# Optimization experiments

Hardware: AMD Instinct MI355X
Metric: run time of the kernel (lower is better)

The kernel has to match this reference:

```python
import jax, jax.numpy as jnp
import numpy as np

INPUT_SIZE = 128
HID = 64
B, T = 256, 1024

def setup_inputs() -> dict:
    key = jax.random.key(0)
    ks = jax.random.split(key, 12)
    s1 = 1.0 / np.sqrt(HID)
    def u(k, shape):
        return jax.random.uniform(k, shape, jnp.float32, -s1, s1)
    return {
        "x": jax.random.normal(ks[0], (B, T, INPUT_SIZE), jnp.float32),
        "w_ih0": u(ks[1], (4 * HID, INPUT_SIZE)),
        "w_hh0": u(ks[2], (4 * HID, HID)),
        "b_ih0": u(ks[3], (4 * HID,)),
        "b_hh0": u(ks[4], (4 * HID,)),
        "w_ih1": u(ks[5], (4 * HID, HID)),
        "w_hh1": u(ks[6], (4 * HID, HID)),
        "b_ih1": u(ks[7], (4 * HID,)),
        "b_hh1": u(ks[8], (4 * HID,)),
        "w_out": u(ks[9], (1, HID)),
        "b_out": u(ks[10], (1,)),
    }

def _lstm(x, w_ih, w_hh, b_ih, b_hh):
    # x: [B, T, I] -> h sequence [B, T, H]; PyTorch gate order i, f, g, o
    Bb = x.shape[0]
    H = w_hh.shape[1]
    # precompute input contribution for all timesteps (one big GEMM)
    xg = jnp.einsum('bti,gi->btg', x, w_ih) + b_ih + b_hh  # [B, T, 4H]
    def step(carry, g_t):
        h, c = carry
        g = g_t + h @ w_hh.T  # [B, 4H]
        i, f, gg, o = jnp.split(g, 4, axis=-1)
        i = jax.nn.sigmoid(i)
        f = jax.nn.sigmoid(f)
        gg = jnp.tanh(gg)
        o = jax.nn.sigmoid(o)
        c = f * c + i * gg
        h = o * jnp.tanh(c)
        return (h, c), h
    init = (jnp.zeros((Bb, H), x.dtype), jnp.zeros((Bb, H), x.dtype))
    _, hs = jax.lax.scan(step, init, jnp.swapaxes(xg, 0, 1))  # [T, B, H]
    return jnp.swapaxes(hs, 0, 1)

def reference(x, w_ih0, w_hh0, b_ih0, b_hh0, w_ih1, w_hh1, b_ih1, b_hh1, w_out, b_out):
    h1 = _lstm(x, w_ih0, w_hh0, b_ih0, b_hh0)   # [B, T, H]
    h2 = _lstm(h1, w_ih1, w_hh1, b_ih1, b_hh1)  # [B, T, H]
    logits = jnp.einsum('bth,oh->bto', h2, w_out) + b_out  # [B, T, 1]
    return jax.nn.sigmoid(logits)
```

## Files before the change

kernel.cpp:

```cpp
#include <hip/hip_runtime.h>

#define BB 256
#define TT 1024
#define II 128
#define HH 64
#define BT (BB * TT)

typedef _Float16 h2 __attribute__((ext_vector_type(2)));
typedef _Float16 half8 __attribute__((ext_vector_type(8)));
typedef float f32x4 __attribute__((ext_vector_type(4)));
typedef unsigned int uint;
typedef unsigned short ushort;

#define DOT2(a, b, c) __builtin_amdgcn_fdot2((a), (b), (c), false)
#define BC(u) __builtin_bit_cast(h2, (uint)(u))
#define MFMA16(a, b, c) __builtin_amdgcn_mfma_f32_16x16x32_f16((a), (b), (c), 0, 0, 0)
#define SIG(v) __builtin_amdgcn_rcpf(1.0f + __expf(-(v)))
#define TNH(v) (1.0f - 2.0f * __builtin_amdgcn_rcpf(1.0f + __expf(2.0f * (v))))

#define BAR() asm volatile("s_waitcnt lgkmcnt(0)\n\ts_barrier" ::: "memory")

#define LDPK(P, ptr) uint P; { float2 _f = *(const float2*)(ptr); \
    h2 _h; _h[0] = (_Float16)_f.x; _h[1] = (_Float16)_f.y; \
    P = __builtin_bit_cast(uint, _h); }
#define PIN8(a,b,c,d,e,f,g,h_) asm volatile("" : "+v"(a),"+v"(b),"+v"(c),"+v"(d),"+v"(e),"+v"(f),"+v"(g),"+v"(h_));
#define LD8(P, base, o) \
    LDPK(P##0,(base)+(o)+ 0) LDPK(P##1,(base)+(o)+ 2) LDPK(P##2,(base)+(o)+ 4) LDPK(P##3,(base)+(o)+ 6) \
    LDPK(P##4,(base)+(o)+ 8) LDPK(P##5,(base)+(o)+10) LDPK(P##6,(base)+(o)+12) LDPK(P##7,(base)+(o)+14) \
    PIN8(P##0,P##1,P##2,P##3,P##4,P##5,P##6,P##7)

#define D8A(P, va, vb, c0, c1, c2, c3) \
    c0 = DOT2(BC(P##0), BC((va).x), c0); c1 = DOT2(BC(P##1), BC((va).y), c1); \
    c2 = DOT2(BC(P##2), BC((va).z), c2); c3 = DOT2(BC(P##3), BC((va).w), c3); \
    c0 = DOT2(BC(P##4), BC((vb).x), c0); c1 = DOT2(BC(P##5), BC((vb).y), c1); \
    c2 = DOT2(BC(P##6), BC((vb).z), c2); c3 = DOT2(BC(P##7), BC((vb).w), c3);

#define GDOT(G, s) { float a0=0.f,a1=0.f,a2=0.f,a3=0.f; \
    D8A(G##A, hv0, hv1, a0,a1,a2,a3) D8A(G##B, hv2, hv3, a0,a1,a2,a3) \
    D8A(G##C, hv4, hv5, a0,a1,a2,a3) D8A(G##D, hv6, hv7, a0,a1,a2,a3) \
    s = (a0 + a1) + (a2 + a3); }

__global__ __launch_bounds__(256)
void xg_mfma(const float* __restrict__ x, const float* __restrict__ w_ih0,
             ushort* __restrict__ xg)
{
    __shared__ __align__(16) _Float16 xt[64][136];
    __shared__ __align__(16) _Float16 wt[128][136];
    const int tid = threadIdx.x, lane = tid & 63, wv = tid >> 6;
    const int bt0 = blockIdx.x * 64;
    {
        const int row = tid >> 2, q = (tid & 3) * 32;
        const float4* src = (const float4*)(x + (size_t)(bt0 + row) * II + q);
        _Float16* dst = &xt[row][q];
        #pragma unroll
        for (int i = 0; i < 8; ++i) {
            float4 v = src[i];
            dst[4*i+0]=(_Float16)v.x; dst[4*i+1]=(_Float16)v.y;
            dst[4*i+2]=(_Float16)v.z; dst[4*i+3]=(_Float16)v.w;
        }
    }
    for (int nh = 0; nh < 2; ++nh) {
        __syncthreads();
        {
            const int n = tid >> 1, kh = (tid & 1) * 64;
            const float4* src = (const float4*)(w_ih0 + (size_t)(nh * 128 + n) * II + kh);
            _Float16* dst = &wt[n][kh];
            #pragma unroll
            for (int i = 0; i < 16; ++i) {
                float4 v = src[i];
                dst[4*i+0]=(_Float16)v.x; dst[4*i+1]=(_Float16)v.y;
                dst[4*i+2]=(_Float16)v.z; dst[4*i+3]=(_Float16)v.w;
            }
        }
        __syncthreads();
        const int m = wv * 16 + (lane & 15);
        const int kf = (lane >> 4) * 8;
        half8 a0 = *(const half8*)&xt[m][ 0 + kf];
        half8 a1 = *(const half8*)&xt[m][32 + kf];
        half8 a2 = *(const half8*)&xt[m][64 + kf];
        half8 a3 = *(const half8*)&xt[m][96 + kf];
        #pragma unroll
        for (int nt = 0; nt < 8; ++nt) {
            const int nloc = nt * 16 + (lane & 15);
            half8 b0 = *(const half8*)&wt[nloc][ 0 + kf];
            half8 b1 = *(const half8*)&wt[nloc][32 + kf];
            half8 b2 = *(const half8*)&wt[nloc][64 + kf];
            half8 b3 = *(const half8*)&wt[nloc][96 + kf];
            f32x4 acc = {0.f, 0.f, 0.f, 0.f};
            acc = MFMA16(a0, b0, acc); acc = MFMA16(a1, b1, acc);
            acc = MFMA16(a2, b2, acc); acc = MFMA16(a3, b3, acc);
            const int col = nh * 128 + nt * 16 + (lane & 15);
            const int idx = (col & 63) * 4 + (col >> 6);
            const int r0  = wv * 16 + (lane >> 4) * 4;
            #pragma unroll
            for (int r = 0; r < 4; ++r) {
                _Float16 hv = (_Float16)acc[r];
                xg[(size_t)(bt0 + r0 + r) * 256 + idx] = __builtin_bit_cast(ushort, hv);
            }
        }
    }
}

__global__ __launch_bounds__(192) __attribute__((amdgpu_waves_per_eu(1, 1)))
void lstm2_core(const float* __restrict__ w_hh0,
                const float* __restrict__ b_ih0, const float* __restrict__ b_hh0,
                const float* __restrict__ w_ih1, const float* __restrict__ w_hh1,
                const float* __restrict__ b_ih1, const float* __restrict__ b_hh1,
                const ushort* __restrict__ xg, ushort* __restrict__ h1g)
{
    const int bb = blockIdx.x;
    const int w  = threadIdx.x >> 6;
    const int j  = threadIdx.x & 63;

    __shared__ __align__(16) uint  h0buf[2][32];
    __shared__ __align__(16) uint  h1buf[2][32];
    __shared__ float zbuf[2][4][68];

    const float* Wsel = (w == 0) ? w_hh0 : (w == 1) ? w_ih1 : w_hh1;
    const float* r0p = Wsel + (size_t)(  0 + j) * 64;
    const float* r1p = Wsel + (size_t)( 64 + j) * 64;
    const float* r2p = Wsel + (size_t)(128 + j) * 64;
    const float* r3p = Wsel + (size_t)(192 + j) * 64;
    LD8(G0A, r0p,  0) LD8(G0B, r0p, 16) LD8(G0C, r0p, 32) LD8(G0D, r0p, 48)
    LD8(G1A, r1p,  0) LD8(G1B, r1p, 16) LD8(G1C, r1p, 32) LD8(G1D, r1p, 48)
    LD8(G2A, r2p,  0) LD8(G2B, r2p, 16) LD8(G2C, r2p, 32) LD8(G2D, r2p, 48)
    LD8(G3A, r3p,  0) LD8(G3B, r3p, 16) LD8(G3C, r3p, 32) LD8(G3D, r3p, 48)

    float bI = 0.f, bF = 0.f, bG = 0.f, bO = 0.f;
    if (w == 0) {
        bI = b_ih0[j]       + b_hh0[j];
        bF = b_ih0[64 + j]  + b_hh0[64 + j];
        bG = b_ih0[128 + j] + b_hh0[128 + j];
        bO = b_ih0[192 + j] + b_hh0[192 + j];
    } else if (w == 2) {
        bI = b_ih1[j]       + b_hh1[j];
        bF = b_ih1[64 + j]  + b_hh1[64 + j];
        bG = b_ih1[128 + j] + b_hh1[128 + j];
        bO = b_ih1[192 + j] + b_hh1[192 + j];
    }

    float cst = 0.0f;
    const ushort* xbase = xg + (size_t)bb * TT * 256 + j * 4;
    ushort* h1b = h1g + (size_t)bb * TT * 64 + j;

    if (threadIdx.x < 32)       h0buf[1][threadIdx.x] = 0u;
    else if (threadIdx.x < 64)  h1buf[1][threadIdx.x - 32] = 0u;
    __syncthreads();

    uint2 xc = {0,0}, xn1 = {0,0}, xn2 = {0,0};
    if (w == 0) {
        xc  = *(const uint2*)(xbase);
        xn1 = *(const uint2*)(xbase + 256);
    }

    for (int k = 0; k < TT + 2; ++k) {
        if (w == 0) {
            if (k + 2 < TT) xn2 = *(const uint2*)(xbase + (size_t)(k + 2) * 256);
            if (k < TT) {
                const uint4* hq = (const uint4*)&h0buf[(k + 1) & 1][0];
                uint4 hv0=hq[0], hv1=hq[1], hv2=hq[2], hv3=hq[3];
                uint4 hv4=hq[4], hv5=hq[5], hv6=hq[6], hv7=hq[7];
                float si, sf, sg, so;
                GDOT(G0, si) GDOT(G1, sf) GDOT(G2, sg) GDOT(G3, so)
                h2 xlo = BC(xc.x), xhi = BC(xc.y);
                si += bI + (float)xlo[0]; sf += bF + (float)xlo[1];
                sg += bG + (float)xhi[0]; so += bO + (float)xhi[1];
                float ii = SIG(si), ff = SIG(sf), gg = TNH(sg), oo = SIG(so);
                cst = fmaf(ff, cst, ii * gg);
                float hval = oo * TNH(cst);
                ((_Float16*)&h0buf[k & 1][0])[j] = (_Float16)hval;
            }
            xc = xn1; xn1 = xn2;
        } else if (w == 1) {
            if (k >= 1 && k <= TT) {
                const int m = k - 1;
                const uint4* hq = (const uint4*)&h0buf[m & 1][0];
                uint4 hv0=hq[0], hv1=hq[1], hv2=hq[2], hv3=hq[3];
                uint4 hv4=hq[4], hv5=hq[5], hv6=hq[6], hv7=hq[7];
                float si, sf, sg, so;
                GDOT(G0, si) GDOT(G1, sf) GDOT(G2, sg) GDOT(G3, so)
                const int s = m & 1;
                zbuf[s][0][j] = si; zbuf[s][1][j] = sf;
                zbuf[s][2][j] = sg; zbuf[s][3][j] = so;
            }
        } else {
            if (k >= 2) {
                const int m = k - 2;
                const int s = m & 1;
                const uint4* hq = (const uint4*)&h1buf[(m + 1) & 1][0];
                uint4 hv0=hq[0], hv1=hq[1], hv2=hq[2], hv3=hq[3];
                uint4 hv4=hq[4], hv5=hq[5], hv6=hq[6], hv7=hq[7];
                float si, sf, sg, so;
                GDOT(G0, si) GDOT(G1, sf) GDOT(G2, sg) GDOT(G3, so)
                si += bI + zbuf[s][0][j]; sf += bF + zbuf[s][1][j];
                sg += bG + zbuf[s][2][j]; so += bO + zbuf[s][3][j];
                float ii = SIG(si), ff = SIG(sf), gg = TNH(sg), oo = SIG(so);
                cst = fmaf(ff, cst, ii * gg);
                float hval = oo * TNH(cst);
                _Float16 hf = (_Float16)hval;
                ((_Float16*)&h1buf[m & 1][0])[j] = hf;
                h1b[(size_t)m * 64] = __builtin_bit_cast(ushort, hf);
            }
        }
        BAR();
    }
}

__global__ __launch_bounds__(256)
void head_gemv(const ushort* __restrict__ h1g, const float* __restrict__ w_out,
               const float* __restrict__ b_out, float* __restrict__ outp)
{
    __shared__ float wsh[64];
    const int tid = threadIdx.x;
    if (tid < 64) wsh[tid] = w_out[tid];
    __syncthreads();
    const int bt = blockIdx.x * 256 + tid;
    const uint4* hp = (const uint4*)(h1g + (size_t)bt * 64);
    float s = 0.0f;
    #pragma unroll
    for (int i = 0; i < 8; ++i) {
        uint4 v = hp[i];
        const float* wp = &wsh[8 * i];
        h2 p;
        p = BC(v.x); s = fmaf((float)p[0], wp[0], s); s = fmaf((float)p[1], wp[1], s);
        p = BC(v.y); s = fmaf((float)p[0], wp[2], s); s = fmaf((float)p[1], wp[3], s);
        p = BC(v.z); s = fmaf((float)p[0], wp[4], s); s = fmaf((float)p[1], wp[5], s);
        p = BC(v.w); s = fmaf((float)p[0], wp[6], s); s = fmaf((float)p[1], wp[7], s);
    }
    outp[bt] = __builtin_amdgcn_rcpf(1.0f + __expf(-(s + b_out[0])));
}

extern "C" void kernel_launch(void* const* d_in, const int* in_sizes, int n_in,
                              void* d_out, int out_size, void* d_ws, size_t ws_size,
                              hipStream_t stream) {
    const float* x     = (const float*)d_in[0];
    const float* w_ih0 = (const float*)d_in[1];
    const float* w_hh0 = (const float*)d_in[2];
    const float* b_ih0 = (const float*)d_in[3];
    const float* b_hh0 = (const float*)d_in[4];
    const float* w_ih1 = (const float*)d_in[5];
    const float* w_hh1 = (const float*)d_in[6];
    const float* b_ih1 = (const float*)d_in[7];
    const float* b_hh1 = (const float*)d_in[8];
    const float* w_out = (const float*)d_in[9];
    const float* b_out = (const float*)d_in[10];
    float* out = (float*)d_out;

    ushort* xg  = (ushort*)d_ws;
    ushort* h1g = (ushort*)((char*)d_ws + (size_t)BT * 256 * 2);

    hipLaunchKernelGGL(xg_mfma, dim3(BT / 64), dim3(256), 0, stream, x, w_ih0, xg);
    hipLaunchKernelGGL(lstm2_core, dim3(BB), dim3(192), 0, stream,
                       w_hh0, b_ih0, b_hh0, w_ih1, w_hh1, b_ih1, b_hh1, xg, h1g);
    hipLaunchKernelGGL(head_gemv, dim3(BT / 256), dim3(256), 0, stream,
                       h1g, w_out, b_out, out);
}
```

Baseline: 822.4 us.

## Prefetch hidden-state and gate vectors into registers across barriers in LSTM core

Restructures the three-wave LSTM pipeline so each wave issues its LDS loads of the next step's hidden vector (and the layer-1 input gates) right after writing, before the barrier. The loads complete under the barrier rather than after it, shortening the per-step critical path. It deepens the ring buffers to four slots, adds pipeline stages, uses partial lgkmcnt waits and barriers without waits per wave, and packs zbuf as float4 per unit. It also changes the xg layout by permuting w_ih0 rows so stores are contiguous. The relaxed waits risk LDS races if the counts or buffer slots are wrong.

```diff
diff --git a/kernel.cpp b/kernel.cpp
--- a/kernel.cpp
+++ b/kernel.cpp
@@ -18,7 +18,9 @@
 #define SIG(v) __builtin_amdgcn_rcpf(1.0f + __expf(-(v)))
 #define TNH(v) (1.0f - 2.0f * __builtin_amdgcn_rcpf(1.0f + __expf(2.0f * (v))))
 
-#define BAR() asm volatile("s_waitcnt lgkmcnt(0)\n\ts_barrier" ::: "memory")
+#define BAR_W8() asm volatile("s_waitcnt lgkmcnt(8)\n\ts_barrier" ::: "memory")
+#define BAR_W0() asm volatile("s_waitcnt lgkmcnt(0)\n\ts_barrier" ::: "memory")
+#define BAR_NP() asm volatile("s_barrier" ::: "memory")
 
 #define LDPK(P, ptr) uint P; { float2 _f = *(const float2*)(ptr); \
     h2 _h; _h[0] = (_Float16)_f.x; _h[1] = (_Float16)_f.y; \
@@ -39,6 +41,10 @@
     D8A(G##A, hv0, hv1, a0,a1,a2,a3) D8A(G##B, hv2, hv3, a0,a1,a2,a3) \
     D8A(G##C, hv4, hv5, a0,a1,a2,a3) D8A(G##D, hv6, hv7, a0,a1,a2,a3) \
     s = (a0 + a1) + (a2 + a3); }
+
+#define LDHV(src) { const uint4* hq_ = (const uint4*)(src); \
+    hv0=hq_[0]; hv1=hq_[1]; hv2=hq_[2]; hv3=hq_[3]; \
+    hv4=hq_[4]; hv5=hq_[5]; hv6=hq_[6]; hv7=hq_[7]; }
 
 __global__ __launch_bounds__(256)
 void xg_mfma(const float* __restrict__ x, const float* __restrict__ w_ih0,
@@ -63,7 +69,9 @@
         __syncthreads();
         {
             const int n = tid >> 1, kh = (tid & 1) * 64;
-            const float4* src = (const float4*)(w_ih0 + (size_t)(nh * 128 + n) * II + kh);
+            const int flatn = nh * 128 + n;
+            const int srcrow = (flatn & 3) * 64 + (flatn >> 2);
+            const float4* src = (const float4*)(w_ih0 + (size_t)srcrow * II + kh);
             _Float16* dst = &wt[n][kh];
             #pragma unroll
             for (int i = 0; i < 16; ++i) {
@@ -89,13 +97,12 @@
             f32x4 acc = {0.f, 0.f, 0.f, 0.f};
             acc = MFMA16(a0, b0, acc); acc = MFMA16(a1, b1, acc);
             acc = MFMA16(a2, b2, acc); acc = MFMA16(a3, b3, acc);
-            const int col = nh * 128 + nt * 16 + (lane & 15);
-            const int idx = (col & 63) * 4 + (col >> 6);
-            const int r0  = wv * 16 + (lane >> 4) * 4;
+            const int colg = nh * 128 + nt * 16 + (lane & 15);
+            const int r0   = wv * 16 + (lane >> 4) * 4;
             #pragma unroll
             for (int r = 0; r < 4; ++r) {
                 _Float16 hv = (_Float16)acc[r];
-                xg[(size_t)(bt0 + r0 + r) * 256 + idx] = __builtin_bit_cast(ushort, hv);
+                xg[(size_t)(bt0 + r0 + r) * 256 + colg] = __builtin_bit_cast(ushort, hv);
             }
         }
     }
@@ -112,9 +119,9 @@
     const int w  = threadIdx.x >> 6;
     const int j  = threadIdx.x & 63;
 
-    __shared__ __align__(16) uint  h0buf[2][32];
-    __shared__ __align__(16) uint  h1buf[2][32];
-    __shared__ float zbuf[2][4][68];
+    __shared__ __align__(16) uint  h0buf[4][32];
+    __shared__ __align__(16) uint  h1buf[32];
+    __shared__ __align__(16) float zbuf[4][64][4];
 
     const float* Wsel = (w == 0) ? w_hh0 : (w == 1) ? w_ih1 : w_hh1;
     const float* r0p = Wsel + (size_t)(  0 + j) * 64;
@@ -143,23 +150,19 @@
     const ushort* xbase = xg + (size_t)bb * TT * 256 + j * 4;
     ushort* h1b = h1g + (size_t)bb * TT * 64 + j;
 
-    if (threadIdx.x < 32)       h0buf[1][threadIdx.x] = 0u;
-    else if (threadIdx.x < 64)  h1buf[1][threadIdx.x - 32] = 0u;
-    __syncthreads();
-
+    uint4 hv0={0,0,0,0}, hv1={0,0,0,0}, hv2={0,0,0,0}, hv3={0,0,0,0};
+    uint4 hv4={0,0,0,0}, hv5={0,0,0,0}, hv6={0,0,0,0}, hv7={0,0,0,0};
+    f32x4 zr = {0.f, 0.f, 0.f, 0.f};
     uint2 xc = {0,0}, xn1 = {0,0}, xn2 = {0,0};
     if (w == 0) {
         xc  = *(const uint2*)(xbase);
         xn1 = *(const uint2*)(xbase + 256);
     }
 
-    for (int k = 0; k < TT + 2; ++k) {
+    for (int k = 0; k < TT + 4; ++k) {
         if (w == 0) {
             if (k + 2 < TT) xn2 = *(const uint2*)(xbase + (size_t)(k + 2) * 256);
             if (k < TT) {
-                const uint4* hq = (const uint4*)&h0buf[(k + 1) & 1][0];
-                uint4 hv0=hq[0], hv1=hq[1], hv2=hq[2], hv3=hq[3];
-                uint4 hv4=hq[4], hv5=hq[5], hv6=hq[6], hv7=hq[7];
                 float si, sf, sg, so;
                 GDOT(G0, si) GDOT(G1, sf) GDOT(G2, sg) GDOT(G3, so)
                 h2 xlo = BC(xc.x), xhi = BC(xc.y);
@@ -168,41 +171,41 @@
                 float ii = SIG(si), ff = SIG(sf), gg = TNH(sg), oo = SIG(so);
                 cst = fmaf(ff, cst, ii * gg);
                 float hval = oo * TNH(cst);
-                ((_Float16*)&h0buf[k & 1][0])[j] = (_Float16)hval;
+                ((_Float16*)&h0buf[k & 3][0])[j] = (_Float16)hval;
+                LDHV(&h0buf[k & 3][0]);
             }
             xc = xn1; xn1 = xn2;
+            BAR_W8();
         } else if (w == 1) {
-            if (k >= 1 && k <= TT) {
-                const int m = k - 1;
-                const uint4* hq = (const uint4*)&h0buf[m & 1][0];
-                uint4 hv0=hq[0], hv1=hq[1], hv2=hq[2], hv3=hq[3];
-                uint4 hv4=hq[4], hv5=hq[5], hv6=hq[6], hv7=hq[7];
+            if (k >= 2 && k < TT + 2) {
+                const int m = k - 2;
                 float si, sf, sg, so;
                 GDOT(G0, si) GDOT(G1, sf) GDOT(G2, sg) GDOT(G3, so)
-                const int s = m & 1;
-                zbuf[s][0][j] = si; zbuf[s][1][j] = sf;
-                zbuf[s][2][j] = sg; zbuf[s][3][j] = so;
-            }
+                f32x4 zv = {si, sf, sg, so};
+                *(f32x4*)&zbuf[m & 3][j][0] = zv;
+            }
+            if (k >= 1 && k <= TT)
+                LDHV(&h0buf[(k - 1) & 3][0]);
+            BAR_W0();
         } else {
-            if (k >= 2) {
-                const int m = k - 2;
-                const int s = m & 1;
-                const uint4* hq = (const uint4*)&h1buf[(m + 1) & 1][0];
-                uint4 hv0=hq[0], hv1=hq[1], hv2=hq[2], hv3=hq[3];
-                uint4 hv4=hq[4], hv5=hq[5], hv6=hq[6], hv7=hq[7];
+            if (k >= 4) {
+                const int m = k - 4;
                 float si, sf, sg, so;
                 GDOT(G0, si) GDOT(G1, sf) GDOT(G2, sg) GDOT(G3, so)
-                si += bI + zbuf[s][0][j]; sf += bF + zbuf[s][1][j];
-                sg += bG + zbuf[s][2][j]; so += bO + zbuf[s][3][j];
+                si += bI + zr[0]; sf += bF + zr[1];
+                sg += bG + zr[2]; so += bO + zr[3];
                 float ii = SIG(si), ff = SIG(sf), gg = TNH(sg), oo = SIG(so);
                 cst = fmaf(ff, cst, ii * gg);
                 float hval = oo * TNH(cst);
                 _Float16 hf = (_Float16)hval;
-                ((_Float16*)&h1buf[m & 1][0])[j] = hf;
+                ((_Float16*)&h1buf[0])[j] = hf;
+                LDHV(&h1buf[0]);
                 h1b[(size_t)m * 64] = __builtin_bit_cast(ushort, hf);
             }
-        }
-        BAR();
+            if (k >= 3 && k < TT + 3)
+                zr = *(const f32x4*)&zbuf[(k - 3) & 3][j][0];
+            BAR_NP();
+        }
     }
 }
 
```

Result: no change. 838.2 us (+1.9%).
